# Kernel tuning notes

Measured on AMD Instinct MI355X. Metric: run time of the kernel, lower is better.

## Reference

```python
import jax, jax.numpy as jnp
import numpy as np

B, N, DIM, H = 4, 2048, 1024, 16
HEAD_DIM = DIM // H
SCALE = HEAD_DIM ** (-0.5)


def setup_inputs() -> dict:
    key = jax.random.key(0)
    k1, k2, k3 = jax.random.split(key, 3)
    x = jax.random.normal(k1, (B, N, DIM), dtype=jnp.float32)
    # nn.Linear(dim, 3*dim, bias=False): weight shape [3*dim, dim], y = x @ W.T
    w_qkv = jax.random.normal(k2, (3 * DIM, DIM), dtype=jnp.float32) * 0.02
    w_proj = jax.random.normal(k3, (DIM, DIM), dtype=jnp.float32) * 0.02
    return {"x": x, "w_qkv": w_qkv, "w_proj": w_proj}


def reference(x, w_qkv, w_proj):
    Bv, Nv, C = x.shape
    Dh = C // H
    # qkv projection -> [B, N, 3, H, Dh]
    qkv = (x @ w_qkv.T).reshape(Bv, Nv, 3, H, Dh)
    q, k, v = qkv[:, :, 0], qkv[:, :, 1], qkv[:, :, 2]  # each [B, N, H, Dh]
    # scaled dot-product attention per head (online-softmax loop collapses to this)
    scores = jnp.einsum("bnhd,bmhd->bhnm", q, k) * SCALE  # [B, H, N, N]
    attn = jax.nn.softmax(scores, axis=-1)
    out = jnp.einsum("bhnm,bmhd->bnhd", attn, v).reshape(Bv, Nv, C)
    return out @ w_proj.T
```

## Files before the change

kernel.cpp:

```cpp
#include <hip/hip_runtime.h>

typedef __bf16 bf16;
typedef bf16 bf16x8 __attribute__((ext_vector_type(8)));
typedef float f32x4 __attribute__((ext_vector_type(4)));
typedef float f32x16 __attribute__((ext_vector_type(16)));
typedef int i32x2 __attribute__((ext_vector_type(2)));

#define B_   4
#define N_   2048
#define DIM_ 1024
#define H_   16
#define DH_  64
#define M_   (B_ * N_)

#define CEXP 0.18033688f

#define GLOBAL_CP(g) (const __attribute__((address_space(1))) void*)(g)
#define LDS_CP(l)    (__attribute__((address_space(3))) void*)(l)

__global__ __launch_bounds__(256) void cvt_all(
    const float* __restrict__ x, const float* __restrict__ wq,
    const float* __restrict__ wp, bf16* __restrict__ o,
    int nx4, int nwq4, int nwp4)
{
    const int i = blockIdx.x * blockDim.x + threadIdx.x;
    const float* src; int si;
    if (i < nx4)                { src = x;  si = i; }
    else if (i < nx4 + nwq4)    { src = wq; si = i - nx4; }
    else                        { src = wp; si = i - nx4 - nwq4; }
    const float4 v = ((const float4*)src)[si];
    union { bf16 h[4]; uint2 u; } r;
    r.h[0] = (bf16)v.x; r.h[1] = (bf16)v.y;
    r.h[2] = (bf16)v.z; r.h[3] = (bf16)v.w;
    ((uint2*)o)[i] = r.u;
}

__global__ __launch_bounds__(256) void gemm_bt(
    const bf16* __restrict__ A, const bf16* __restrict__ Bm,
    int Ndim, int K, int mode,
    float* __restrict__ outf,
    bf16* __restrict__ qb, bf16* __restrict__ kbv, bf16* __restrict__ vbT)
{
    __shared__ bf16 As[128 * 64];
    __shared__ bf16 Bs[128 * 64];

    const int tid  = threadIdx.x;
    const int wave = tid >> 6;
    const int lane = tid & 63;
    const int quad = lane >> 4;
    const int lr   = lane & 15;
    const int wr   = wave >> 1, wc = wave & 1;
    const int m0 = blockIdx.y * 128;
    const int n0 = blockIdx.x * 128;

    f32x4 acc[4][4];
#pragma unroll
    for (int i = 0; i < 4; i++)
#pragma unroll
        for (int j = 0; j < 4; j++) acc[i][j] = f32x4{0.f, 0.f, 0.f, 0.f};

    const int sl8 = lane >> 3;
    const int sc8 = ((lane & 7) ^ (sl8 & 7)) * 8;

    for (int k0 = 0; k0 < K; k0 += 64) {
        __syncthreads();
#pragma unroll
        for (int c = 0; c < 4; c++) {
            const int ii  = wave * 4 + c;
            const int row = ii * 8 + sl8;
            __builtin_amdgcn_global_load_lds(
                GLOBAL_CP(A + (size_t)(m0 + row) * K + k0 + sc8),
                LDS_CP(&As[ii * 512 + lane * 8]), 16, 0, 0);
            __builtin_amdgcn_global_load_lds(
                GLOBAL_CP(Bm + (size_t)(n0 + row) * K + k0 + sc8),
                LDS_CP(&Bs[ii * 512 + lane * 8]), 16, 0, 0);
        }
        __syncthreads();

#pragma unroll
        for (int s = 0; s < 2; s++) {
            bf16x8 af[4], bfr[4];
#pragma unroll
            for (int i = 0; i < 4; i++) {
                const int R = wr * 64 + i * 16 + lr;
                af[i] = *(const bf16x8*)(&As[R * 64 + (((s * 4 + quad) ^ (R & 7)) << 3)]);
            }
#pragma unroll
            for (int j = 0; j < 4; j++) {
                const int R = wc * 64 + j * 16 + lr;
                bfr[j] = *(const bf16x8*)(&Bs[R * 64 + (((s * 4 + quad) ^ (R & 7)) << 3)]);
            }
#pragma unroll
            for (int i = 0; i < 4; i++)
#pragma unroll
                for (int j = 0; j < 4; j++)
                    acc[i][j] = __builtin_amdgcn_mfma_f32_16x16x32_bf16(
                        af[i], bfr[j], acc[i][j], 0, 0, 0);
        }
    }

#pragma unroll
    for (int i = 0; i < 4; i++) {
        const int mbase = m0 + wr * 64 + i * 16 + quad * 4;
#pragma unroll
        for (int j = 0; j < 4; j++) {
            const int n = n0 + wc * 64 + j * 16 + lr;
            if (mode == 0) {
#pragma unroll
                for (int r = 0; r < 4; r++)
                    outf[(size_t)(mbase + r) * Ndim + n] = acc[i][j][r];
            } else {
                const int which = n >> 10;
                const int h = (n >> 6) & 15;
                const int d = n & 63;
                const int b  = mbase >> 11;
                const int t0 = mbase & 2047;
                if (which == 2) {
                    union { uint2 u; bf16 hh[4]; } p;
#pragma unroll
                    for (int r = 0; r < 4; r++) p.hh[r] = (bf16)acc[i][j][r];
                    *(uint2*)(&vbT[(((size_t)(b * 16 + h)) * 64 + d) * 2048 + t0]) = p.u;
                } else {
                    bf16* dst = (which == 0) ? qb : kbv;
                    const float sc = (which == 0) ? CEXP : 1.0f;
#pragma unroll
                    for (int r = 0; r < 4; r++)
                        dst[(((size_t)(b * 16 + h)) * 2048 + t0 + r) * 64 + d] =
                            (bf16)(acc[i][j][r] * sc);
                }
            }
        }
    }
}

__global__ __launch_bounds__(256, 4) void attn_kernel(
    const bf16* __restrict__ qb, const bf16* __restrict__ kb,
    const bf16* __restrict__ vbT, bf16* __restrict__ ao)
{
    __shared__ bf16 Ks[128 * 64];
    __shared__ bf16 Vs[64 * 128];

    const int tid  = threadIdx.x;
    const int wave = tid >> 6;
    const int lane = tid & 63;
    const int l31  = lane & 31;
    const int hh   = lane >> 5;

    const int bid = blockIdx.x;
    const int qt  = (bid >> 3) & 15;
    const int bh  = ((bid >> 7) << 3) | (bid & 7);

    const bf16* Q  = qb  + (size_t)bh * N_ * DH_;
    const bf16* Kp = kb  + (size_t)bh * N_ * DH_;
    const bf16* Vp = vbT + (size_t)bh * DH_ * N_;

    bf16x8 qf[4];
#pragma unroll
    for (int ks = 0; ks < 4; ks++)
        qf[ks] = *(const bf16x8*)(Q + (size_t)(qt * 128 + wave * 32 + l31) * DH_
                                    + ks * 16 + hh * 8);

    bf16x8 onesb;
#pragma unroll
    for (int j = 0; j < 8; j++) onesb[j] = (bf16)1.0f;

    const int krow0 = (lane >> 3);
    const int kscol = ((lane & 7) ^ ((lane >> 3) & 7)) * 8;
    const int vrow0 = (lane >> 4);

    f32x16 oacc[2];
    f32x16 sacc;
#pragma unroll
    for (int r = 0; r < 16; r++) { oacc[0][r] = 0.f; oacc[1][r] = 0.f; sacc[r] = 0.f; }

    for (int t = 0; t < N_ / 128; t++) {
        __syncthreads();
#pragma unroll
        for (int c = 0; c < 4; c++) {
            const int ii = wave * 4 + c;
            const int krow = ii * 8 + krow0;
            __builtin_amdgcn_global_load_lds(
                GLOBAL_CP(Kp + (size_t)(t * 128 + krow) * DH_ + kscol),
                LDS_CP(&Ks[ii * 512 + lane * 8]), 16, 0, 0);
            const int vrow = ii * 4 + vrow0;
            const int vscol = ((lane & 15) ^ (vrow & 15)) * 8;
            __builtin_amdgcn_global_load_lds(
                GLOBAL_CP(Vp + (size_t)vrow * N_ + t * 128 + vscol),
                LDS_CP(&Vs[ii * 512 + lane * 8]), 16, 0, 0);
        }
        __syncthreads();

#pragma unroll
        for (int kbk = 0; kbk < 4; kbk++) {
            f32x16 e;
#pragma unroll
            for (int r = 0; r < 16; r++) e[r] = 0.f;
#pragma unroll
            for (int ks = 0; ks < 4; ks++) {
                const int R  = kbk * 32 + l31;
                const int ch = ks * 2 + hh;
                bf16x8 ak = *(const bf16x8*)(&Ks[R * 64 + ((ch ^ (R & 7)) << 3)]);
                e = __builtin_amdgcn_mfma_f32_32x32x16_bf16(ak, qf[ks], e, 0, 0, 0);
            }

#pragma unroll
            for (int r = 0; r < 16; r++) e[r] = exp2f(e[r]);

            uint g[8];
#pragma unroll
            for (int m = 0; m < 8; m++) {
                union { uint u; bf16 h2[2]; } pk;
                pk.h2[0] = (bf16)e[2 * m];
                pk.h2[1] = (bf16)e[2 * m + 1];
                g[m] = pk.u;
            }

            const i32x2 s0 = __builtin_amdgcn_permlane32_swap((int)g[0], (int)g[2], false, false);
            const i32x2 s1 = __builtin_amdgcn_permlane32_swap((int)g[1], (int)g[3], false, false);
            const i32x2 s2 = __builtin_amdgcn_permlane32_swap((int)g[4], (int)g[6], false, false);
            const i32x2 s3 = __builtin_amdgcn_permlane32_swap((int)g[5], (int)g[7], false, false);

            union { uint u[4]; bf16x8 v; } p0u, p1u;
            p0u.u[0] = (uint)s0[0];
            p0u.u[1] = (uint)s1[0];
            p0u.u[2] = (uint)s0[1];
            p0u.u[3] = (uint)s1[1];
            p1u.u[0] = (uint)s2[0];
            p1u.u[1] = (uint)s3[0];
            p1u.u[2] = (uint)s2[1];
            p1u.u[3] = (uint)s3[1];

            sacc = __builtin_amdgcn_mfma_f32_32x32x16_bf16(p0u.v, onesb, sacc, 0, 0, 0);
            sacc = __builtin_amdgcn_mfma_f32_32x32x16_bf16(p1u.v, onesb, sacc, 0, 0, 0);

#pragma unroll
            for (int dblk = 0; dblk < 2; dblk++) {
                const int R   = dblk * 32 + l31;
                const int ch0 = kbk * 4 + hh;
                const int ch1 = kbk * 4 + 2 + hh;
                bf16x8 bv0 = *(const bf16x8*)(&Vs[R * 128 + ((ch0 ^ (R & 15)) << 3)]);
                bf16x8 bv1 = *(const bf16x8*)(&Vs[R * 128 + ((ch1 ^ (R & 15)) << 3)]);
                oacc[dblk] = __builtin_amdgcn_mfma_f32_32x32x16_bf16(p0u.v, bv0, oacc[dblk], 0, 0, 0);
                oacc[dblk] = __builtin_amdgcn_mfma_f32_32x32x16_bf16(p1u.v, bv1, oacc[dblk], 0, 0, 0);
            }
        }
    }

    const int head = bh & 15;
    const int b    = bh >> 4;
#pragma unroll
    for (int r = 0; r < 16; r++) {
        const int qr  = (r & 3) + 8 * (r >> 2) + 4 * hh;
        const float inv = 1.0f / sacc[r];
        const int qrow = qt * 128 + wave * 32 + qr;
#pragma unroll
        for (int dblk = 0; dblk < 2; dblk++)
            ao[((size_t)(b * 2048 + qrow)) * 1024 + head * 64 + dblk * 32 + l31] =
                (bf16)(oacc[dblk][r] * inv);
    }
}

extern "C" void kernel_launch(void* const* d_in, const int* in_sizes, int n_in,
                              void* d_out, int out_size, void* d_ws, size_t ws_size,
                              hipStream_t stream)
{
    const float* x     = (const float*)d_in[0];
    const float* wqkv  = (const float*)d_in[1];
    const float* wproj = (const float*)d_in[2];
    float* out = (float*)d_out;

    const size_t nx  = (size_t)M_ * DIM_;
    const size_t nwq = (size_t)3 * DIM_ * DIM_;
    const size_t nwp = (size_t)DIM_ * DIM_;
    const size_t seg = (size_t)B_ * H_ * N_ * DH_;

    bf16* xb     = (bf16*)d_ws;
    bf16* wqkvb  = xb + nx;
    bf16* wprojb = wqkvb + nwq;
    bf16* qb     = wprojb + nwp;
    bf16* kb     = qb + seg;
    bf16* vbT    = kb + seg;
    bf16* ao     = xb;

    const int nx4  = (int)(nx / 4), nwq4 = (int)(nwq / 4), nwp4 = (int)(nwp / 4);
    cvt_all<<<(nx4 + nwq4 + nwp4) / 256, 256, 0, stream>>>(
        x, wqkv, wproj, xb, nx4, nwq4, nwp4);

    gemm_bt<<<dim3(24, 64), 256, 0, stream>>>(xb, wqkvb, 3 * DIM_, DIM_, 1,
                                              nullptr, qb, kb, vbT);
    attn_kernel<<<dim3(1024), 256, 0, stream>>>(qb, kb, vbT, ao);
    gemm_bt<<<dim3(8, 64), 256, 0, stream>>>(ao, wprojb, DIM_, DIM_, 0,
                                             out, nullptr, nullptr, nullptr);
}
```

Measured before the change: 294.2 us.

## Double-buffer K/V tiles in attention kernel with 64-key stages

Halves the per-iteration K/V tile from 128 to 64 keys and ping-pongs between two LDS buffers. The next tile's async global-to-LDS load is issued before computing on the current one, leaving one barrier per iteration instead of two. This is meant to overlap memory latency with MFMA work. LDS use stays the same, but twice as many iterations mean more loop and barrier overhead. There is no explicit vmcnt wait before the barrier, so correctness depends on the compiler inserting waits for the async loads.

```diff
diff --git a/kernel.cpp b/kernel.cpp
--- a/kernel.cpp
+++ b/kernel.cpp
@@ -137,8 +137,8 @@
     const bf16* __restrict__ qb, const bf16* __restrict__ kb,
     const bf16* __restrict__ vbT, bf16* __restrict__ ao)
 {
-    __shared__ bf16 Ks[128 * 64];
-    __shared__ bf16 Vs[64 * 128];
+    __shared__ bf16 Ks[2][64 * 64];
+    __shared__ bf16 Vs[2][64 * 64];
 
     const int tid  = threadIdx.x;
     const int wave = tid >> 6;
@@ -164,34 +164,38 @@
 #pragma unroll
     for (int j = 0; j < 8; j++) onesb[j] = (bf16)1.0f;
 
-    const int krow0 = (lane >> 3);
-    const int kscol = ((lane & 7) ^ ((lane >> 3) & 7)) * 8;
-    const int vrow0 = (lane >> 4);
+    const int srow = lane >> 3;
+    const int scol = ((lane & 7) ^ (srow & 7)) * 8;
 
     f32x16 oacc[2];
     f32x16 sacc;
 #pragma unroll
     for (int r = 0; r < 16; r++) { oacc[0][r] = 0.f; oacc[1][r] = 0.f; sacc[r] = 0.f; }
 
-    for (int t = 0; t < N_ / 128; t++) {
-        __syncthreads();
-#pragma unroll
-        for (int c = 0; c < 4; c++) {
-            const int ii = wave * 4 + c;
-            const int krow = ii * 8 + krow0;
-            __builtin_amdgcn_global_load_lds(
-                GLOBAL_CP(Kp + (size_t)(t * 128 + krow) * DH_ + kscol),
-                LDS_CP(&Ks[ii * 512 + lane * 8]), 16, 0, 0);
-            const int vrow = ii * 4 + vrow0;
-            const int vscol = ((lane & 15) ^ (vrow & 15)) * 8;
-            __builtin_amdgcn_global_load_lds(
-                GLOBAL_CP(Vp + (size_t)vrow * N_ + t * 128 + vscol),
-                LDS_CP(&Vs[ii * 512 + lane * 8]), 16, 0, 0);
-        }
-        __syncthreads();
-
-#pragma unroll
-        for (int kbk = 0; kbk < 4; kbk++) {
+#define STAGE(t, pb)                                                          \
+    do {                                                                      \
+        _Pragma("unroll")                                                     \
+        for (int c = 0; c < 2; c++) {                                         \
+            const int ii  = wave * 2 + c;                           \
+            const int row = ii * 8 + srow;                         \
+            __builtin_amdgcn_global_load_lds(                                 \
+                GLOBAL_CP(Kp + (size_t)((t) * 64 + row) * DH_ + scol),        \
+                LDS_CP(&Ks[pb][ii * 512 + lane * 8]), 16, 0, 0);              \
+            __builtin_amdgcn_global_load_lds(                                 \
+                GLOBAL_CP(Vp + (size_t)row * N_ + (t) * 64 + scol),           \
+                LDS_CP(&Vs[pb][ii * 512 + lane * 8]), 16, 0, 0);              \
+        }                                                                     \
+    } while (0)
+
+    STAGE(0, 0);
+    __syncthreads();
+
+    int cur = 0;
+    for (int t = 0; t < N_ / 64; t++) {
+        if (t + 1 < N_ / 64) STAGE(t + 1, cur ^ 1);
+
+#pragma unroll
+        for (int kbk = 0; kbk < 2; kbk++) {
             f32x16 e;
 #pragma unroll
             for (int r = 0; r < 16; r++) e[r] = 0.f;
@@ -199,7 +203,7 @@
             for (int ks = 0; ks < 4; ks++) {
                 const int R  = kbk * 32 + l31;
                 const int ch = ks * 2 + hh;
-                bf16x8 ak = *(const bf16x8*)(&Ks[R * 64 + ((ch ^ (R & 7)) << 3)]);
+                bf16x8 ak = *(const bf16x8*)(&Ks[cur][R * 64 + ((ch ^ (R & 7)) << 3)]);
                 e = __builtin_amdgcn_mfma_f32_32x32x16_bf16(ak, qf[ks], e, 0, 0, 0);
             }
 
@@ -238,13 +242,17 @@
                 const int R   = dblk * 32 + l31;
                 const int ch0 = kbk * 4 + hh;
                 const int ch1 = kbk * 4 + 2 + hh;
-                bf16x8 bv0 = *(const bf16x8*)(&Vs[R * 128 + ((ch0 ^ (R & 15)) << 3)]);
-                bf16x8 bv1 = *(const bf16x8*)(&Vs[R * 128 + ((ch1 ^ (R & 15)) << 3)]);
+                bf16x8 bv0 = *(const bf16x8*)(&Vs[cur][R * 64 + ((ch0 ^ (R & 7)) << 3)]);
+                bf16x8 bv1 = *(const bf16x8*)(&Vs[cur][R * 64 + ((ch1 ^ (R & 7)) << 3)]);
                 oacc[dblk] = __builtin_amdgcn_mfma_f32_32x32x16_bf16(p0u.v, bv0, oacc[dblk], 0, 0, 0);
                 oacc[dblk] = __builtin_amdgcn_mfma_f32_32x32x16_bf16(p1u.v, bv1, oacc[dblk], 0, 0, 0);
             }
         }
+
+        __syncthreads();
+        cur ^= 1;
     }
+#undef STAGE
 
     const int head = bh & 15;
     const int b    = bh >> 4;
```

Measured after the change: 299.7 us. Within noise of the previous version (+1.9%).
